# Optimization experiments

Measured on AMD Instinct MI355X. Metric: run time of the kernel, lower is better.

Reference implementation:

```python
import jax, jax.numpy as jnp
import numpy as np

N = 50000   # nodes
E = 800000  # edges (avg degree 16)
G = 32      # graphs in batch
IN = 128; HID = 64; H = 2; C = 16
NEG_SLOPE = 0.2
BN_EPS = 1e-5


def setup_inputs() -> dict:
    key = jax.random.key(0)
    ks = jax.random.split(key, 16)
    def rn(k, shape, scale=0.1):
        return jax.random.normal(k, shape, jnp.float32) * scale
    return {
        "feat": jax.random.normal(ks[0], (N, IN), jnp.float32),
        "W0": rn(ks[1], (IN, H * HID)),
        "attn0": rn(ks[2], (H, HID)),
        "W1": rn(ks[3], (H * HID, H * HID)),
        "attn1": rn(ks[4], (H, HID)),
        "W2": rn(ks[5], (H * HID, H * HID)),
        "attn2": rn(ks[6], (H, HID)),
        "Wf": rn(ks[7], (H * HID, H * C)),
        "attnf": rn(ks[8], (H, C)),
        "mlp_w1": rn(ks[9], (C, C)),
        "mlp_gamma": jnp.ones((C,), jnp.float32),
        "mlp_beta": jnp.zeros((C,), jnp.float32),
        "mlp_w2": rn(ks[10], (C, C)),
        "src": jax.random.randint(ks[11], (E,), 0, N, jnp.int32),
        "dst": jax.random.randint(ks[12], (E,), 0, N, jnp.int32),
        "node_graph": jnp.sort(jax.random.randint(ks[13], (N,), 0, G, jnp.int32)),
        "num_graphs": G,
    }


def gatv2_layer(h, src, dst, W, attn, act):
    """DGL GATv2Conv with share_weights=True, bias=False, residual=False."""
    n = h.shape[0]
    nh, d = attn.shape
    z = (h @ W).reshape(n, nh, d)                      # [N,H,D]
    zs = z[src]                                        # [E,H,D] gather (src)
    e = jax.nn.leaky_relu(zs + z[dst], NEG_SLOPE)      # [E,H,D]
    score = jnp.einsum('ehd,hd->eh', e, attn)          # [E,H]
    # edge softmax over incoming edges of dst (shift-invariant max trick)
    m = jax.lax.stop_gradient(jax.ops.segment_max(score, dst, num_segments=n))
    a = jnp.exp(score - m[dst])
    denom = jax.ops.segment_sum(a, dst, num_segments=n)[dst]
    alpha = a / jnp.where(denom == 0, 1.0, denom)      # [E,H]
    out = jax.ops.segment_sum(alpha[..., None] * zs, dst, num_segments=n)  # [N,H,D]
    return act(out) if act is not None else out


def reference(feat, W0, attn0, W1, attn1, W2, attn2, Wf, attnf,
              mlp_w1, mlp_gamma, mlp_beta, mlp_w2,
              src, dst, node_graph, num_graphs):
    relu = jax.nn.relu
    n = feat.shape[0]
    h = gatv2_layer(feat, src, dst, W0, attn0, relu).reshape(n, -1)
    h = gatv2_layer(h, src, dst, W1, attn1, relu).reshape(n, -1)
    h = gatv2_layer(h, src, dst, W2, attn2, relu).reshape(n, -1)
    logits = gatv2_layer(h, src, dst, Wf, attnf, None).mean(axis=1)  # [N,C]
    pooled = jax.ops.segment_sum(logits, node_graph, num_segments=num_graphs)  # [G,C]
    # MLP: relu(batchnorm(lin0(x))) -> lin1 (training-mode batch stats, biased var)
    h1 = pooled @ mlp_w1
    mu = h1.mean(axis=0)
    var = h1.var(axis=0)
    h1 = (h1 - mu) / jnp.sqrt(var + BN_EPS) * mlp_gamma + mlp_beta
    out = relu(h1) @ mlp_w2
    return jax.nn.log_softmax(out, axis=-1)
```

## Files before the change

kernel.cpp:

```cpp
#include <hip/hip_runtime.h>
#include <hip/hip_bf16.h>
#include <hip/hip_fp16.h>
#include <math.h>

#define NN 50000
#define EE 800000
#define GG 32
#define HD 64
#define NHEAD 2
#define CCLS 16
#define NEG_SLOPE 0.2f
#define BN_EPS 1e-5f
#define LOG2E 1.4426950408889634f
#define STRIDE 64

typedef unsigned int u32;
typedef unsigned short u16;
typedef _Float16 hv2 __attribute__((ext_vector_type(2)));
typedef __fp16   cv2 __attribute__((ext_vector_type(2)));

__device__ __forceinline__ hv2 bch2(u32 u) { union { u32 u; hv2 h; } c; c.u = u; return c.h; }
__device__ __forceinline__ u32 pkrtz(float a, float b) {
    cv2 r = __builtin_amdgcn_cvt_pkrtz(a, b);
    union { cv2 h; u32 u; } c; c.h = r; return c.u;
}
__device__ __forceinline__ hv2 h2max(hv2 a, hv2 b) {
    return __builtin_elementwise_max(a, b);
}
__device__ __forceinline__ float fdot2(hv2 a, hv2 b, float c) {
#if __has_builtin(__builtin_amdgcn_fdot2)
    union { hv2 h; cv2 c2; } ua, ub;
    ua.h = a; ub.h = b;
    return __builtin_amdgcn_fdot2(ua.c2, ub.c2, c, false);
#else
    return fmaf((float)a[0], (float)b[0], fmaf((float)a[1], (float)b[1], c));
#endif
}


__global__ __launch_bounds__(256) void scatter_kernel(const int* __restrict__ src,
                                                      const int* __restrict__ dst,
                                                      int* __restrict__ cursor,
                                                      u16* __restrict__ csr_src) {
    int e = blockIdx.x * 256 + threadIdx.x;
    if (e < EE) {
        int d = dst[e];
        int s = src[e];
        int p = atomicAdd(&cursor[d], 1);
        csr_src[d * STRIDE + p] = (u16)s;
    }
}


template<int KOUT, int RPT, bool F16IN>
__device__ __forceinline__ void gemm_body(const void* __restrict__ hv,
                                          const float* __restrict__ W,
                                          u32* __restrict__ z, int n, int blk) {
    constexpr int CT = KOUT / 8;
    constexpr int RT = 256 / CT;
    constexpr int BR = RT * RPT;
    constexpr int WSTR = (KOUT == 128) ? 140 : (KOUT + 4);
    __shared__ __align__(16) u32 WpD[64 * WSTR];
    __shared__ __align__(16) uint4 hsU4[BR * 17];
    int t = threadIdx.x;
    int row0 = blk * BR;

    for (int i = t; i < 64 * (KOUT / 4); i += 256) {
        int k2 = i / (KOUT / 4), cq = i % (KOUT / 4);
        float4 wa = ((const float4*)W)[(2 * k2) * (KOUT / 4) + cq];
        float4 wb = ((const float4*)W)[(2 * k2 + 1) * (KOUT / 4) + cq];
        uint4 d;
        d.x = pkrtz(wa.x, wb.x); d.y = pkrtz(wa.y, wb.y);
        d.z = pkrtz(wa.z, wb.z); d.w = pkrtz(wa.w, wb.w);
        *(uint4*)&WpD[k2 * WSTR + 4 * cq + ((cq >> 3) << 2)] = d;
    }
    for (int i = t; i < BR * 16; i += 256) {
        int r = i >> 4, c16 = i & 15;
        int gr = row0 + r;
        uint4 u = {0, 0, 0, 0};
        if (gr < n) {
            if (F16IN) {
                u = ((const uint4*)hv)[(size_t)gr * 16 + c16];
            } else {
                float4 f0 = ((const float4*)hv)[(size_t)gr * 32 + 2 * c16];
                float4 f1 = ((const float4*)hv)[(size_t)gr * 32 + 2 * c16 + 1];
                u.x = pkrtz(f0.x, f0.y); u.y = pkrtz(f0.z, f0.w);
                u.z = pkrtz(f1.x, f1.y); u.w = pkrtz(f1.z, f1.w);
            }
        }
        hsU4[r * 17 + c16] = u;
    }
    __syncthreads();

    int tc = t % CT, tr = t / CT;
    float acc[RPT][8];
    #pragma unroll
    for (int i = 0; i < RPT; i++)
        #pragma unroll
        for (int c = 0; c < 8; c++) acc[i][c] = 0.f;

    for (int kq = 0; kq < 16; kq++) {
        uint4 a4[RPT];
        #pragma unroll
        for (int i = 0; i < RPT; i++) a4[i] = hsU4[(tr * RPT + i) * 17 + kq];
        #pragma unroll
        for (int j = 0; j < 4; j++) {
            const u32* wrow = &WpD[(4 * kq + j) * WSTR + tc * 8 + ((tc >> 2) << 2)];
            uint4 wa = *(const uint4*)wrow;
            uint4 wb = *(const uint4*)(wrow + 4);
            u32 wd[8] = {wa.x, wa.y, wa.z, wa.w, wb.x, wb.y, wb.z, wb.w};
            #pragma unroll
            for (int i = 0; i < RPT; i++) {
                u32 av[4] = {a4[i].x, a4[i].y, a4[i].z, a4[i].w};
                hv2 a2 = bch2(av[j]);
                #pragma unroll
                for (int c = 0; c < 8; c++)
                    acc[i][c] = fdot2(a2, bch2(wd[c]), acc[i][c]);
            }
        }
    }
    #pragma unroll
    for (int i = 0; i < RPT; i++) {
        int gr = row0 + tr * RPT + i;
        if (gr < n) {
            uint4 p;
            p.x = pkrtz(acc[i][0], acc[i][1]);
            p.y = pkrtz(acc[i][2], acc[i][3]);
            p.z = pkrtz(acc[i][4], acc[i][5]);
            p.w = pkrtz(acc[i][6], acc[i][7]);
            ((uint4*)z)[(size_t)gr * (KOUT / 8) + tc] = p;
        }
    }
}

template<int KOUT, int RPT, bool F16IN>
__global__ __launch_bounds__(256) void gemm_kernel(const void* __restrict__ hv,
                                                   const float* __restrict__ W,
                                                   u32* __restrict__ z, int n) {
    gemm_body<KOUT, RPT, F16IN>(hv, W, z, n, blockIdx.x);
}


__global__ __launch_bounds__(256) void edge_kernel(const u32* __restrict__ z,
                                                   const float* __restrict__ attn,
                                                   const int* __restrict__ cursor,
                                                   const u16* __restrict__ csr_src,
                                                   u32* __restrict__ out, int n) {
    int wave = blockIdx.x * 4 + (threadIdx.x >> 6);
    int lane = threadIdx.x & 63;
    if (wave >= n) return;
    int i = wave;
    int slot = lane >> 3;
    int q8 = lane & 7;
    const uint4* zr = (const uint4*)z;

    size_t rowi = (size_t)i * 16 + q8 * 2;
    uint4 zua = zr[rowi], zub = zr[rowi + 1];
    hv2 zd[8] = {bch2(zua.x), bch2(zua.y), bch2(zua.z), bch2(zua.w),
                 bch2(zub.x), bch2(zub.y), bch2(zub.z), bch2(zub.w)};
    const float4* af = (const float4*)attn;
    float4 a0 = af[q8 * 4 + 0], a1 = af[q8 * 4 + 1];
    float4 a2 = af[q8 * 4 + 2], a3 = af[q8 * 4 + 3];
    hv2 ah[8] = {bch2(pkrtz(a0.x * LOG2E, a0.y * LOG2E)),
                 bch2(pkrtz(a0.z * LOG2E, a0.w * LOG2E)),
                 bch2(pkrtz(a1.x * LOG2E, a1.y * LOG2E)),
                 bch2(pkrtz(a1.z * LOG2E, a1.w * LOG2E)),
                 bch2(pkrtz(a2.x * LOG2E, a2.y * LOG2E)),
                 bch2(pkrtz(a2.z * LOG2E, a2.w * LOG2E)),
                 bch2(pkrtz(a3.x * LOG2E, a3.y * LOG2E)),
                 bch2(pkrtz(a3.z * LOG2E, a3.w * LOG2E))};
    const hv2 slope2 = {(_Float16)NEG_SLOPE, (_Float16)NEG_SLOPE};

    int deg = cursor[i];
    const u16* ep = csr_src + i * STRIDE;

    float s = 0.f;
    float accf[16];
    #pragma unroll
    for (int j = 0; j < 16; j++) accf[j] = 0.f;

    bool valid = slot < deg;
    int sid = valid ? (int)ep[slot] : i;
    size_t rs = (size_t)sid * 16 + q8 * 2;
    uint4 sa = zr[rs], sb = zr[rs + 1];

    for (int k = 0; k < deg; k += 8) {
        bool more = (k + 8) < deg;
        bool v2 = (k + 8 + slot) < deg;
        uint4 na, nb;
        if (more) {
            int sid2 = v2 ? (int)ep[k + 8 + slot] : i;
            size_t rs2 = (size_t)sid2 * 16 + q8 * 2;
            na = zr[rs2]; nb = zr[rs2 + 1];
        }
        hv2 zs[8] = {bch2(sa.x), bch2(sa.y), bch2(sa.z), bch2(sa.w),
                     bch2(sb.x), bch2(sb.y), bch2(sb.z), bch2(sb.w)};
        float sc = 0.f;
        #pragma unroll
        for (int j = 0; j < 8; j++) {
            hv2 x = zs[j] + zd[j];
            x = h2max(x, x * slope2);
            sc = fdot2(x, ah[j], sc);
        }
        sc += __shfl_xor(sc, 2, 64);
        sc += __shfl_xor(sc, 1, 64);
        float p = valid ? exp2f(sc) : 0.f;
        s += p;
        #pragma unroll
        for (int j = 0; j < 8; j++) {
            accf[2 * j]     = fmaf(p, (float)zs[j][0], accf[2 * j]);
            accf[2 * j + 1] = fmaf(p, (float)zs[j][1], accf[2 * j + 1]);
        }
        sa = na; sb = nb; valid = v2;
    }

    #pragma unroll
    for (int off = 8; off <= 32; off <<= 1) {
        s += __shfl_xor(s, off, 64);
        #pragma unroll
        for (int j = 0; j < 16; j++) accf[j] += __shfl_xor(accf[j], off, 64);
    }

    if (slot == 0) {
        float inv = s > 0.f ? 1.f / s : 0.f;
        float o[16];
        #pragma unroll
        for (int j = 0; j < 16; j++) o[j] = fmaxf(accf[j] * inv, 0.f);
        uint4 pa, pb;
        pa.x = pkrtz(o[0], o[1]);   pa.y = pkrtz(o[2], o[3]);
        pa.z = pkrtz(o[4], o[5]);   pa.w = pkrtz(o[6], o[7]);
        pb.x = pkrtz(o[8], o[9]);   pb.y = pkrtz(o[10], o[11]);
        pb.z = pkrtz(o[12], o[13]); pb.w = pkrtz(o[14], o[15]);
        ((uint4*)out)[rowi] = pa;
        ((uint4*)out)[rowi + 1] = pb;
    }
}


__global__ __launch_bounds__(256) void edge_final_kernel(const u32* __restrict__ z,
                                                         const float* __restrict__ attn,
                                                         const int* __restrict__ cursor,
                                                         const u16* __restrict__ csr_src,
                                                         float* __restrict__ logits, int n) {
    int wave = blockIdx.x * 4 + (threadIdx.x >> 6);
    int lane = threadIdx.x & 63;
    int iv = wave * 2 + (lane >> 5);
    bool mine = iv < n;
    int i = mine ? iv : (n - 1);
    int hl = lane & 31;
    int j = hl >> 3;
    int d8 = hl & 7;
    const uint2* zr = (const uint2*)z;
    uint2 zu = zr[(size_t)i * 8 + d8];
    hv2 zd0 = bch2(zu.x), zd1 = bch2(zu.y);
    float4 av = ((const float4*)attn)[d8];
    hv2 ah0 = bch2(pkrtz(av.x * LOG2E, av.y * LOG2E));
    hv2 ah1 = bch2(pkrtz(av.z * LOG2E, av.w * LOG2E));
    const hv2 slope2 = {(_Float16)NEG_SLOPE, (_Float16)NEG_SLOPE};
    int deg = cursor[i];
    const u16* ep = csr_src + i * STRIDE;

    float s = 0.f;
    float accf[4] = {0.f, 0.f, 0.f, 0.f};
    for (int k = 0; k < deg; k += 4) {
        int kk = k + j;
        bool valid = kk < deg;
        int sid = valid ? (int)ep[kk] : i;
        uint2 su = zr[(size_t)sid * 8 + d8];
        hv2 zs0 = bch2(su.x), zs1 = bch2(su.y);
        hv2 x;
        float sc = 0.f;
        x = zs0 + zd0; x = h2max(x, x * slope2); sc = fdot2(x, ah0, sc);
        x = zs1 + zd1; x = h2max(x, x * slope2); sc = fdot2(x, ah1, sc);
        sc += __shfl_xor(sc, 1, 64);
        sc += __shfl_xor(sc, 2, 64);
        float p = valid ? exp2f(sc) : 0.f;
        s += p;
        accf[0] = fmaf(p, (float)zs0[0], accf[0]);
        accf[1] = fmaf(p, (float)zs0[1], accf[1]);
        accf[2] = fmaf(p, (float)zs1[0], accf[2]);
        accf[3] = fmaf(p, (float)zs1[1], accf[3]);
    }
    #pragma unroll
    for (int off = 8; off <= 16; off <<= 1) {
        s += __shfl_xor(s, off, 64);
        #pragma unroll
        for (int jj = 0; jj < 4; jj++) accf[jj] += __shfl_xor(accf[jj], off, 64);
    }
    float inv = s > 0.f ? 1.f / s : 0.f;
    float4 o;
    o.x = accf[0] * inv; o.y = accf[1] * inv; o.z = accf[2] * inv; o.w = accf[3] * inv;
    o.x = 0.5f * (o.x + __shfl_xor(o.x, 4, 64));
    o.y = 0.5f * (o.y + __shfl_xor(o.y, 4, 64));
    o.z = 0.5f * (o.z + __shfl_xor(o.z, 4, 64));
    o.w = 0.5f * (o.w + __shfl_xor(o.w, 4, 64));
    if (mine && j == 0 && (hl & 4) == 0)
        ((float4*)logits)[i * 4 + (hl & 3)] = o;
}


__global__ __launch_bounds__(256) void pool_kernel(const float* __restrict__ logits,
                                                   const int* __restrict__ node_graph,
                                                   float* __restrict__ pooled) {
    int t = threadIdx.x;
    int c = t & 15;
    int ci = t >> 4;
    int start = blockIdx.x * 1024 + ci * 64;
    float acc = 0.f;
    int gcur = -1;
    for (int j = 0; j < 64; j++) {
        int node = start + j;
        if (node >= NN) break;
        int g = node_graph[node];
        if (g != gcur) {
            if (gcur >= 0) atomicAdd(&pooled[gcur * 16 + c], acc);
            gcur = g; acc = 0.f;
        }
        acc += logits[node * 16 + c];
    }
    if (gcur >= 0) atomicAdd(&pooled[gcur * 16 + c], acc);
}


__global__ __launch_bounds__(512) void mlp_kernel(const float* __restrict__ pooled,
                                                  const float* __restrict__ w1,
                                                  const float* __restrict__ gamma,
                                                  const float* __restrict__ beta,
                                                  const float* __restrict__ w2,
                                                  float* __restrict__ out) {
    __shared__ float P[GG * CCLS], H1[GG * CCLS], H2[GG * CCLS], O[GG * CCLS];
    __shared__ float mu[CCLS], rstd[CCLS], rowm[GG], rowl[GG];
    int t = threadIdx.x;
    int r = t >> 4, c = t & 15;
    if (t < GG * CCLS) P[t] = pooled[t];
    __syncthreads();
    if (t < GG * CCLS) {
        float s = 0.f;
        for (int k = 0; k < 16; k++) s += P[r * 16 + k] * w1[k * 16 + c];
        H1[t] = s;
    }
    __syncthreads();
    if (t < CCLS) {
        float s = 0.f;
        for (int rr = 0; rr < GG; rr++) s += H1[rr * 16 + t];
        float mn = s / GG;
        float s2 = 0.f;
        for (int rr = 0; rr < GG; rr++) { float d = H1[rr * 16 + t] - mn; s2 += d * d; }
        mu[t] = mn; rstd[t] = rsqrtf(s2 / GG + BN_EPS);
    }
    __syncthreads();
    if (t < GG * CCLS) {
        float v = (H1[t] - mu[c]) * rstd[c] * gamma[c] + beta[c];
        H2[t] = fmaxf(v, 0.f);
    }
    __syncthreads();
    if (t < GG * CCLS) {
        float s = 0.f;
        for (int k = 0; k < 16; k++) s += H2[r * 16 + k] * w2[k * 16 + c];
        O[t] = s;
    }
    __syncthreads();
    if (t < GG) {
        float mx = -INFINITY;
        for (int k = 0; k < 16; k++) mx = fmaxf(mx, O[t * 16 + k]);
        float l = 0.f;
        for (int k = 0; k < 16; k++) l += __expf(O[t * 16 + k] - mx);
        rowm[t] = mx; rowl[t] = logf(l);
    }
    __syncthreads();
    if (t < GG * CCLS) out[t] = O[t] - rowm[r] - rowl[r];
}


extern "C" void kernel_launch(void* const* d_in, const int* in_sizes, int n_in,
                              void* d_out, int out_size, void* d_ws, size_t ws_size,
                              hipStream_t stream) {
    const float* feat     = (const float*)d_in[0];
    const float* W0       = (const float*)d_in[1];
    const float* attn0    = (const float*)d_in[2];
    const float* W1       = (const float*)d_in[3];
    const float* attn1    = (const float*)d_in[4];
    const float* W2       = (const float*)d_in[5];
    const float* attn2    = (const float*)d_in[6];
    const float* Wf       = (const float*)d_in[7];
    const float* attnf    = (const float*)d_in[8];
    const float* mlp_w1   = (const float*)d_in[9];
    const float* mlp_g    = (const float*)d_in[10];
    const float* mlp_b    = (const float*)d_in[11];
    const float* mlp_w2   = (const float*)d_in[12];
    const int*   src      = (const int*)d_in[13];
    const int*   dst      = (const int*)d_in[14];
    const int*   ngraph   = (const int*)d_in[15];
    float* out = (float*)d_out;

    char* ws = (char*)d_ws;
    size_t off = 0;
    auto alloc = [&](size_t bytes) {
        void* p = ws + off;
        off = (off + bytes + 255) & ~(size_t)255;
        return p;
    };
    u32* z      = (u32*)alloc((size_t)NN * 64 * sizeof(u32));
    u32* hb0    = (u32*)alloc((size_t)NN * 64 * sizeof(u32));
    u32* hb1    = (u32*)alloc((size_t)NN * 64 * sizeof(u32));
    float* logits = (float*)alloc((size_t)NN * 16 * sizeof(float));
    float* pooled = (float*)alloc(GG * CCLS * sizeof(float));
    int* cursor   = (int*)alloc(NN * sizeof(int));
    u16* csr_src  = (u16*)alloc((size_t)NN * STRIDE * sizeof(u16));

    hipMemsetAsync(cursor, 0, NN * sizeof(int), stream);
    hipMemsetAsync(pooled, 0, GG * CCLS * sizeof(float), stream);

    int edge_grid = (NN + 3) / 4;
    int edgef_grid = (NN + 7) / 8;
    int gemm_grid = (NN + 63) / 64;
    int scat_grid = (EE + 255) / 256;

    gemm_kernel<128, 4, false><<<gemm_grid, 256, 0, stream>>>(feat, W0, z, NN);
    scatter_kernel<<<scat_grid, 256, 0, stream>>>(src, dst, cursor, csr_src);
    edge_kernel<<<edge_grid, 256, 0, stream>>>(z, attn0, cursor, csr_src, hb0, NN);

    gemm_kernel<128, 4, true><<<gemm_grid, 256, 0, stream>>>(hb0, W1, z, NN);
    edge_kernel<<<edge_grid, 256, 0, stream>>>(z, attn1, cursor, csr_src, hb1, NN);

    gemm_kernel<128, 4, true><<<gemm_grid, 256, 0, stream>>>(hb1, W2, z, NN);
    edge_kernel<<<edge_grid, 256, 0, stream>>>(z, attn2, cursor, csr_src, hb0, NN);

    gemm_kernel<32, 1, true><<<gemm_grid, 256, 0, stream>>>(hb0, Wf, z, NN);
    edge_final_kernel<<<edgef_grid, 256, 0, stream>>>(z, attnf, cursor, csr_src, logits, NN);

    pool_kernel<<<(NN + 1023) / 1024, 256, 0, stream>>>(logits, ngraph, pooled);
    mlp_kernel<<<1, 512, 0, stream>>>(pooled, mlp_w1, mlp_g, mlp_b, mlp_w2, out);
}
```

Measured before the change: 429.7 us.

## Two-pass bucketed CSR build to localize scatter atomics by destination

```diff
diff --git a/kernel.cpp b/kernel.cpp
--- a/kernel.cpp
+++ b/kernel.cpp
@@ -13,9 +13,12 @@
 #define BN_EPS 1e-5f
 #define LOG2E 1.4426950408889634f
 #define STRIDE 64
+#define BUCKCAP 110000
+#define SLICES 392
 
 typedef unsigned int u32;
 typedef unsigned short u16;
+typedef unsigned long long u64;
 typedef _Float16 hv2 __attribute__((ext_vector_type(2)));
 typedef __fp16   cv2 __attribute__((ext_vector_type(2)));
 
@@ -38,14 +41,49 @@
 }
 
 
-__global__ __launch_bounds__(256) void scatter_kernel(const int* __restrict__ src,
-                                                      const int* __restrict__ dst,
-                                                      int* __restrict__ cursor,
-                                                      u16* __restrict__ csr_src) {
+__global__ __launch_bounds__(256) void bucket_kernel(const int* __restrict__ src,
+                                                     const int* __restrict__ dst,
+                                                     int* __restrict__ bcur,
+                                                     u32* __restrict__ buckets) {
     int e = blockIdx.x * 256 + threadIdx.x;
+    int lane = threadIdx.x & 63;
+    int mybucket = 8;
+    u32 pk = 0;
     if (e < EE) {
         int d = dst[e];
         int s = src[e];
+        mybucket = d & 7;
+        pk = ((u32)d << 16) | (u32)s;
+    }
+    #pragma unroll
+    for (int b = 0; b < 8; b++) {
+        u64 m = __ballot(mybucket == b);
+        if (m == 0ull) continue;
+        int cnt = __popcll(m);
+        int leader = __ffsll((long long)m) - 1;
+        int base = 0;
+        if (lane == leader) base = atomicAdd(&bcur[b], cnt);
+        base = __shfl(base, leader, 64);
+        if (mybucket == b) {
+            int rank = __popcll(m & ((1ull << lane) - 1ull));
+            buckets[b * BUCKCAP + base + rank] = pk;
+        }
+    }
+}
+
+
+__global__ __launch_bounds__(256) void scatter2_kernel(const u32* __restrict__ buckets,
+                                                       const int* __restrict__ bcur,
+                                                       int* __restrict__ cursor,
+                                                       u16* __restrict__ csr_src) {
+    int b = blockIdx.x & 7;
+    int slice = blockIdx.x >> 3;
+    int cnt = bcur[b];
+    const u32* bp = buckets + b * BUCKCAP;
+    for (int idx = slice * 256 + threadIdx.x; idx < cnt; idx += SLICES * 256) {
+        u32 pk = bp[idx];
+        int d = pk >> 16;
+        int s = pk & 0xffff;
         int p = atomicAdd(&cursor[d], 1);
         csr_src[d * STRIDE + p] = (u16)s;
     }
@@ -405,19 +443,22 @@
     u32* hb1    = (u32*)alloc((size_t)NN * 64 * sizeof(u32));
     float* logits = (float*)alloc((size_t)NN * 16 * sizeof(float));
     float* pooled = (float*)alloc(GG * CCLS * sizeof(float));
-    int* cursor   = (int*)alloc(NN * sizeof(int));
+    int* cursor   = (int*)alloc((NN + 8) * sizeof(int));
+    int* bcur     = cursor + NN;
     u16* csr_src  = (u16*)alloc((size_t)NN * STRIDE * sizeof(u16));
-
-    hipMemsetAsync(cursor, 0, NN * sizeof(int), stream);
+    u32* buckets  = (u32*)alloc((size_t)8 * BUCKCAP * sizeof(u32));
+
+    hipMemsetAsync(cursor, 0, (NN + 8) * sizeof(int), stream);
     hipMemsetAsync(pooled, 0, GG * CCLS * sizeof(float), stream);
 
     int edge_grid = (NN + 3) / 4;
     int edgef_grid = (NN + 7) / 8;
     int gemm_grid = (NN + 63) / 64;
-    int scat_grid = (EE + 255) / 256;
+    int buck_grid = (EE + 255) / 256;
 
     gemm_kernel<128, 4, false><<<gemm_grid, 256, 0, stream>>>(feat, W0, z, NN);
-    scatter_kernel<<<scat_grid, 256, 0, stream>>>(src, dst, cursor, csr_src);
+    bucket_kernel<<<buck_grid, 256, 0, stream>>>(src, dst, bcur, buckets);
+    scatter2_kernel<<<8 * SLICES, 256, 0, stream>>>(buckets, bcur, cursor, csr_src);
     edge_kernel<<<edge_grid, 256, 0, stream>>>(z, attn0, cursor, csr_src, hb0, NN);
 
     gemm_kernel<128, 4, true><<<gemm_grid, 256, 0, stream>>>(hb0, W1, z, NN);
```

Result: slower. 1.565 ms (+264.2%).

## Fuse memsets into first GEMM, pooling into final edge kernel, fp16 shuffle reduce

Applied to the files above, without the earlier changes.

```diff
diff --git a/kernel.cpp b/kernel.cpp
--- a/kernel.cpp
+++ b/kernel.cpp
@@ -20,6 +20,7 @@
 typedef __fp16   cv2 __attribute__((ext_vector_type(2)));
 
 __device__ __forceinline__ hv2 bch2(u32 u) { union { u32 u; hv2 h; } c; c.u = u; return c.h; }
+__device__ __forceinline__ u32 bcu32(hv2 h) { union { hv2 h; u32 u; } c; c.h = h; return c.u; }
 __device__ __forceinline__ u32 pkrtz(float a, float b) {
     cv2 r = __builtin_amdgcn_cvt_pkrtz(a, b);
     union { cv2 h; u32 u; } c; c.h = r; return c.u;
@@ -138,6 +139,17 @@
                                                    const float* __restrict__ W,
                                                    u32* __restrict__ z, int n) {
     gemm_body<KOUT, RPT, F16IN>(hv, W, z, n, blockIdx.x);
+}
+
+__global__ __launch_bounds__(256) void gemm0_kernel(const void* __restrict__ hv,
+                                                    const float* __restrict__ W,
+                                                    u32* __restrict__ z,
+                                                    int* __restrict__ cursor,
+                                                    float* __restrict__ pooled) {
+    int gid = blockIdx.x * 256 + threadIdx.x;
+    if (gid < NN) cursor[gid] = 0;
+    if (gid < GG * CCLS) pooled[gid] = 0.f;
+    gemm_body<128, 4, false>(hv, W, z, NN, blockIdx.x);
 }
 
 
@@ -214,23 +226,32 @@
         sa = na; sb = nb; valid = v2;
     }
 
+    u32 pk[8];
+    #pragma unroll
+    for (int j = 0; j < 8; j++) pk[j] = pkrtz(accf[2 * j], accf[2 * j + 1]);
     #pragma unroll
     for (int off = 8; off <= 32; off <<= 1) {
         s += __shfl_xor(s, off, 64);
         #pragma unroll
-        for (int j = 0; j < 16; j++) accf[j] += __shfl_xor(accf[j], off, 64);
+        for (int j = 0; j < 8; j++) {
+            u32 o = (u32)__shfl_xor((int)pk[j], off, 64);
+            pk[j] = bcu32(bch2(pk[j]) + bch2(o));
+        }
     }
 
     if (slot == 0) {
         float inv = s > 0.f ? 1.f / s : 0.f;
-        float o[16];
-        #pragma unroll
-        for (int j = 0; j < 16; j++) o[j] = fmaxf(accf[j] * inv, 0.f);
+        hv2 inv2 = bch2(pkrtz(inv, inv));
+        const hv2 zero2 = {(_Float16)0.f, (_Float16)0.f};
         uint4 pa, pb;
-        pa.x = pkrtz(o[0], o[1]);   pa.y = pkrtz(o[2], o[3]);
-        pa.z = pkrtz(o[4], o[5]);   pa.w = pkrtz(o[6], o[7]);
-        pb.x = pkrtz(o[8], o[9]);   pb.y = pkrtz(o[10], o[11]);
-        pb.z = pkrtz(o[12], o[13]); pb.w = pkrtz(o[14], o[15]);
+        pa.x = bcu32(h2max(bch2(pk[0]) * inv2, zero2));
+        pa.y = bcu32(h2max(bch2(pk[1]) * inv2, zero2));
+        pa.z = bcu32(h2max(bch2(pk[2]) * inv2, zero2));
+        pa.w = bcu32(h2max(bch2(pk[3]) * inv2, zero2));
+        pb.x = bcu32(h2max(bch2(pk[4]) * inv2, zero2));
+        pb.y = bcu32(h2max(bch2(pk[5]) * inv2, zero2));
+        pb.z = bcu32(h2max(bch2(pk[6]) * inv2, zero2));
+        pb.w = bcu32(h2max(bch2(pk[7]) * inv2, zero2));
         ((uint4*)out)[rowi] = pa;
         ((uint4*)out)[rowi + 1] = pb;
     }
@@ -241,7 +262,12 @@
                                                          const float* __restrict__ attn,
                                                          const int* __restrict__ cursor,
                                                          const u16* __restrict__ csr_src,
-                                                         float* __restrict__ logits, int n) {
+                                                         const int* __restrict__ node_graph,
+                                                         float* __restrict__ pooled, int n) {
+    __shared__ float pl[GG * CCLS];
+    for (int t = threadIdx.x; t < GG * CCLS; t += 256) pl[t] = 0.f;
+    __syncthreads();
+
     int wave = blockIdx.x * 4 + (threadIdx.x >> 6);
     int lane = threadIdx.x & 63;
     int iv = wave * 2 + (lane >> 5);
@@ -294,31 +320,19 @@
     o.y = 0.5f * (o.y + __shfl_xor(o.y, 4, 64));
     o.z = 0.5f * (o.z + __shfl_xor(o.z, 4, 64));
     o.w = 0.5f * (o.w + __shfl_xor(o.w, 4, 64));
-    if (mine && j == 0 && (hl & 4) == 0)
-        ((float4*)logits)[i * 4 + (hl & 3)] = o;
-}
-
-
-__global__ __launch_bounds__(256) void pool_kernel(const float* __restrict__ logits,
-                                                   const int* __restrict__ node_graph,
-                                                   float* __restrict__ pooled) {
-    int t = threadIdx.x;
-    int c = t & 15;
-    int ci = t >> 4;
-    int start = blockIdx.x * 1024 + ci * 64;
-    float acc = 0.f;
-    int gcur = -1;
-    for (int j = 0; j < 64; j++) {
-        int node = start + j;
-        if (node >= NN) break;
-        int g = node_graph[node];
-        if (g != gcur) {
-            if (gcur >= 0) atomicAdd(&pooled[gcur * 16 + c], acc);
-            gcur = g; acc = 0.f;
-        }
-        acc += logits[node * 16 + c];
-    }
-    if (gcur >= 0) atomicAdd(&pooled[gcur * 16 + c], acc);
+    if (mine && j == 0 && (hl & 4) == 0) {
+        int g = node_graph[i];
+        float* base = &pl[g * 16 + 4 * d8];
+        atomicAdd(&base[0], o.x);
+        atomicAdd(&base[1], o.y);
+        atomicAdd(&base[2], o.z);
+        atomicAdd(&base[3], o.w);
+    }
+    __syncthreads();
+    for (int t = threadIdx.x; t < GG * CCLS; t += 256) {
+        float v = pl[t];
+        if (v != 0.f) atomicAdd(&pooled[t], v);
+    }
 }
 
 
@@ -403,20 +417,16 @@
     u32* z      = (u32*)alloc((size_t)NN * 64 * sizeof(u32));
     u32* hb0    = (u32*)alloc((size_t)NN * 64 * sizeof(u32));
     u32* hb1    = (u32*)alloc((size_t)NN * 64 * sizeof(u32));
-    float* logits = (float*)alloc((size_t)NN * 16 * sizeof(float));
     float* pooled = (float*)alloc(GG * CCLS * sizeof(float));
     int* cursor   = (int*)alloc(NN * sizeof(int));
     u16* csr_src  = (u16*)alloc((size_t)NN * STRIDE * sizeof(u16));
-
-    hipMemsetAsync(cursor, 0, NN * sizeof(int), stream);
-    hipMemsetAsync(pooled, 0, GG * CCLS * sizeof(float), stream);
 
     int edge_grid = (NN + 3) / 4;
     int edgef_grid = (NN + 7) / 8;
     int gemm_grid = (NN + 63) / 64;
     int scat_grid = (EE + 255) / 256;
 
-    gemm_kernel<128, 4, false><<<gemm_grid, 256, 0, stream>>>(feat, W0, z, NN);
+    gemm0_kernel<<<gemm_grid, 256, 0, stream>>>(feat, W0, z, cursor, pooled);
     scatter_kernel<<<scat_grid, 256, 0, stream>>>(src, dst, cursor, csr_src);
     edge_kernel<<<edge_grid, 256, 0, stream>>>(z, attn0, cursor, csr_src, hb0, NN);
 
@@ -427,8 +437,8 @@
     edge_kernel<<<edge_grid, 256, 0, stream>>>(z, attn2, cursor, csr_src, hb0, NN);
 
     gemm_kernel<32, 1, true><<<gemm_grid, 256, 0, stream>>>(hb0, Wf, z, NN);
-    edge_final_kernel<<<edgef_grid, 256, 0, stream>>>(z, attnf, cursor, csr_src, logits, NN);
-
-    pool_kernel<<<(NN + 1023) / 1024, 256, 0, stream>>>(logits, ngraph, pooled);
+    edge_final_kernel<<<edgef_grid, 256, 0, stream>>>(z, attnf, cursor, csr_src,
+                                                      ngraph, pooled, NN);
+
     mlp_kernel<<<1, 512, 0, stream>>>(pooled, mlp_w1, mlp_g, mlp_b, mlp_w2, out);
 }
```

New measurement: 399.9 us. -6.9%, faster.
